# Kernel tuning notes

Measured on AMD Instinct MI355X. Metric: run time of the kernel, lower is better.

## Reference

```python
import jax, jax.numpy as jnp
import numpy as np

HC = 4
C = 2048
TMAX = 8
RMS_EPS = 1e-6
PRE_EPS = 1e-4
SINK_EPS = 1e-6
POST_MULT = 2.0


def setup_inputs() -> dict:
    key = jax.random.key(0)
    k1, k2, k3 = jax.random.split(key, 3)
    B, S = 2, 2048
    x = jax.random.normal(k1, (B, S, HC, C), dtype=jnp.float32)
    phi = jax.random.normal(k2, (HC * C, HC * HC + 2 * HC), dtype=jnp.float32) * 0.02
    b = jnp.zeros((HC * HC + 2 * HC,), dtype=jnp.float32)
    alpha_pre = jnp.ones((), dtype=jnp.float32)
    alpha_post = jnp.ones((), dtype=jnp.float32)
    alpha_res = jnp.ones((), dtype=jnp.float32)
    W = jax.random.normal(k3, (C, C), dtype=jnp.float32) * 0.02
    Wb = jnp.zeros((C,), dtype=jnp.float32)
    return {"x": x, "phi": phi, "b": b, "alpha_pre": alpha_pre,
            "alpha_post": alpha_post, "alpha_res": alpha_res, "W": W, "Wb": Wb}


def _coeffs(x, phi, b, alpha_pre, alpha_post, alpha_res):
    # x: [..., hc, c] -> flatten streams, RMSNorm over k = hc*c
    lead = x.shape[:-2]
    flat = x.reshape(lead + (HC * C,))
    xn = flat * jax.lax.rsqrt(jnp.mean(flat * flat, axis=-1, keepdims=True) + RMS_EPS)
    logits = xn @ phi + b  # [..., hc*hc + 2*hc]
    pre = logits[..., :HC]
    post = logits[..., HC:2 * HC]
    res = logits[..., 2 * HC:].reshape(lead + (HC, HC))
    h_pre = jax.nn.sigmoid(alpha_pre * pre) + PRE_EPS          # [..., hc]
    h_post = POST_MULT * jax.nn.sigmoid(alpha_post * post)     # [..., hc]
    # Sinkhorn normalization -> approximately doubly-stochastic hc x hc matrix
    M = jnp.exp(alpha_res * res)

    def step(m, _):
        m = m / (jnp.sum(m, axis=-1, keepdims=True) + SINK_EPS)
        m = m / (jnp.sum(m, axis=-2, keepdims=True) + SINK_EPS)
        return m, None

    h_res, _ = jax.lax.scan(step, M, None, length=TMAX)
    return h_pre, h_post, h_res


def reference(x, phi, b, alpha_pre, alpha_post, alpha_res, W, Wb):
    xf = x.astype(jnp.float32)
    h_pre, h_post, h_res = _coeffs(xf, phi, b, alpha_pre, alpha_post, alpha_res)
    # combine streams into single layer input: [..., c]
    x_in = jnp.sum(xf * h_pre[..., None], axis=-2)
    f_out = x_in @ W + Wb  # the wrapped layer (Linear)
    # residual stream mixing + broadcasted post-scaled layer output
    x_out = jnp.einsum('...oi,...ic->...oc', h_res, xf) + h_post[..., None] * f_out[..., None, :]
    return x_out.astype(x.dtype)
```

## Files before the change

### kernel.cpp

```cpp
#include <hip/hip_runtime.h>
#include <hip/hip_bf16.h>

#define HCn 4
#define Cn 2048
#define Dn (HCn*Cn)
#define NLg 24
#define TMAXn 8

typedef short bf16x8 __attribute__((ext_vector_type(8)));
typedef float f32x4 __attribute__((ext_vector_type(4)));

__device__ __forceinline__ unsigned int pk2(float a, float b) {
  union { __hip_bfloat162 h; unsigned int u; } v;
  v.h = __float22bfloat162_rn(float2{a, b});
  return v.u;
}
__device__ __forceinline__ float sigm(float z) { return 1.0f / (1.0f + expf(-z)); }

__device__ __forceinline__ void gload_lds16(const void* g, void* l) {
  __builtin_amdgcn_global_load_lds((__attribute__((address_space(1))) void*)(g),
                                   (__attribute__((address_space(3))) void*)(l),
                                   16, 0, 0);
}

__global__ __launch_bounds__(128) void phib_kernel(const float* __restrict__ phi,
                                                   unsigned short* __restrict__ phiB) {
  int tid = threadIdx.x;
  int nt = tid >> 6, lane = tid & 63;
  int ks = blockIdx.x;
  int col = nt * 16 + (lane & 15);
  int kb = ks * 32 + (lane >> 4) * 8;
  float v[8];
#pragma unroll
  for (int e = 0; e < 8; ++e)
    v[e] = (col < NLg) ? phi[(size_t)(kb + e) * NLg + col] : 0.f;
  uint4 o = { pk2(v[0], v[1]), pk2(v[2], v[3]), pk2(v[4], v[5]), pk2(v[6], v[7]) };
  *(uint4*)&phiB[((size_t)(ks * 2 + nt) * 64 + lane) * 8] = o;
}

__global__ __launch_bounds__(512) void logits_kernel(
    const float* __restrict__ x, const unsigned short* __restrict__ phiB,
    float* __restrict__ pbuf) {
  __shared__ float lgp[8][16][33];
  __shared__ float ssp[8][16];

  int tid = threadIdx.x, lane = tid & 63, wid = tid >> 6;
  int g = blockIdx.x >> 2;
  int kc = blockIdx.x & 3;
  long t0 = (long)g * 16;
  int l15 = lane & 15, kg = lane >> 4;

  int kbase = kc * 2048 + wid * 256;
  const float* xr = x + (size_t)(t0 + l15) * Dn + kbase + kg * 8;
  const bf16x8* pB = (const bf16x8*)phiB + (size_t)(kbase >> 5) * 128 + lane;

  float ss = 0.f;
  f32x4 acc0 = {0.f,0.f,0.f,0.f}, acc1 = {0.f,0.f,0.f,0.f};

  float4 A0[3], A1[3]; bf16x8 Bv0[3], Bv1[3];
#define LOADIT(IT, S) {                          \
    A0[S] = *(const float4*)(xr + (IT) * 32);    \
    A1[S] = *(const float4*)(xr + (IT) * 32 + 4);\
    Bv0[S] = pB[(IT) * 128];                     \
    Bv1[S] = pB[(IT) * 128 + 64]; }
#define PROCIT(S) {                                                           \
    float4 P0 = A0[S], P1 = A1[S];                                            \
    ss += P0.x*P0.x + P0.y*P0.y + P0.z*P0.z + P0.w*P0.w;                      \
    ss += P1.x*P1.x + P1.y*P1.y + P1.z*P1.z + P1.w*P1.w;                      \
    uint4 u_ = { pk2(P0.x,P0.y), pk2(P0.z,P0.w), pk2(P1.x,P1.y), pk2(P1.z,P1.w) }; \
    bf16x8 a_ = *(bf16x8*)&u_;                                                \
    acc0 = __builtin_amdgcn_mfma_f32_16x16x32_bf16(a_, Bv0[S], acc0, 0, 0, 0);\
    acc1 = __builtin_amdgcn_mfma_f32_16x16x32_bf16(a_, Bv1[S], acc1, 0, 0, 0); }

  LOADIT(0, 0); LOADIT(1, 1);
#pragma unroll
  for (int it = 0; it < 8; ++it) {
    if (it < 6) LOADIT(it + 2, (it + 2) % 3);
    PROCIT(it % 3);
  }
#undef LOADIT
#undef PROCIT

  ss += __shfl_xor(ss, 16); ss += __shfl_xor(ss, 32);
  if (kg == 0) ssp[wid][l15] = ss;
#pragma unroll
  for (int e = 0; e < 4; ++e) {
    int tok = kg * 4 + e;
    lgp[wid][tok][l15] = acc0[e];
    lgp[wid][tok][16 + l15] = acc1[e];
  }
  __syncthreads();

  for (int q = tid; q < 16 * 25; q += 512) {
    int tk = q / 25, j = q % 25;
    float v = 0.f;
    if (j < 24) {
#pragma unroll
      for (int w = 0; w < 8; ++w) v += lgp[w][tk][j];
    } else {
#pragma unroll
      for (int w = 0; w < 8; ++w) v += ssp[w][tk];
    }
    pbuf[(size_t)(t0 + tk) * 100 + kc * 25 + j] = v;
  }
}

__global__ __launch_bounds__(256) void finalize_kernel(
    const float* __restrict__ pbuf, const float* __restrict__ bb,
    const float* __restrict__ apre_p, const float* __restrict__ apost_p,
    const float* __restrict__ ares_p, float* __restrict__ hpre,
    float* __restrict__ hpost, float* __restrict__ hres) {
  long t = (long)blockIdx.x * 256 + threadIdx.x;
  const float* pt = pbuf + (size_t)t * 100;
  float lg[25];
#pragma unroll
  for (int j = 0; j < 25; ++j)
    lg[j] = pt[j] + pt[25 + j] + pt[50 + j] + pt[75 + j];
  float r = rsqrtf(lg[24] / (float)Dn + 1e-6f);
  float apre = apre_p[0], apost = apost_p[0], ares = ares_p[0];
#pragma unroll
  for (int j = 0; j < NLg; ++j) lg[j] = r * lg[j] + bb[j];
#pragma unroll
  for (int j = 0; j < 4; ++j) hpre[t * 4 + j] = sigm(apre * lg[j]) + 1e-4f;
#pragma unroll
  for (int j = 0; j < 4; ++j) hpost[t * 4 + j] = 2.0f * sigm(apost * lg[4 + j]);
  float m[16];
#pragma unroll
  for (int q = 0; q < 16; ++q) m[q] = expf(ares * lg[8 + q]);
  for (int it = 0; it < TMAXn; ++it) {
#pragma unroll
    for (int o = 0; o < 4; ++o) {
      float rs = m[o*4] + m[o*4+1] + m[o*4+2] + m[o*4+3] + 1e-6f;
      m[o*4] /= rs; m[o*4+1] /= rs; m[o*4+2] /= rs; m[o*4+3] /= rs;
    }
#pragma unroll
    for (int i = 0; i < 4; ++i) {
      float cs = m[i] + m[4+i] + m[8+i] + m[12+i] + 1e-6f;
      m[i] /= cs; m[4+i] /= cs; m[8+i] /= cs; m[12+i] /= cs;
    }
  }
#pragma unroll
  for (int q = 0; q < 16; ++q) hres[t * 16 + q] = m[q];
}

__global__ __launch_bounds__(256) void xin_kernel(
    const float* __restrict__ x, const float* __restrict__ hpre,
    unsigned int* __restrict__ xin) {
  long t = blockIdx.x;
  int tid = threadIdx.x;
  float h0 = hpre[t * 4 + 0], h1 = hpre[t * 4 + 1];
  float h2 = hpre[t * 4 + 2], h3 = hpre[t * 4 + 3];
  const float4* xt = (const float4*)(x + (size_t)t * Dn);
  uint2* xo = (uint2*)xin + (size_t)t * (Cn / 4);
#pragma unroll
  for (int it = 0; it < 2; ++it) {
    int c4 = it * 256 + tid;
    float4 v0 = xt[c4];
    float4 v1 = xt[c4 + 512];
    float4 v2 = xt[c4 + 1024];
    float4 v3 = xt[c4 + 1536];
    float sx = h0*v0.x + h1*v1.x + h2*v2.x + h3*v3.x;
    float sy = h0*v0.y + h1*v1.y + h2*v2.y + h3*v3.y;
    float sz = h0*v0.z + h1*v1.z + h2*v2.z + h3*v3.z;
    float sw = h0*v0.w + h1*v1.w + h2*v2.w + h3*v3.w;
    uint2 o; o.x = pk2(sx, sy); o.y = pk2(sz, sw);
    xo[c4] = o;
  }
}

__global__ __launch_bounds__(256) void wtrans_kernel(const float* __restrict__ W,
                                                     unsigned short* __restrict__ Wt) {
  __shared__ float tile[64][65];
  int kb = blockIdx.y * 64, nb = blockIdx.x * 64;
  int tr = threadIdx.x >> 4;
  int tc = threadIdx.x & 15;
#pragma unroll
  for (int rr = 0; rr < 64; rr += 16) {
    float4 v = *(const float4*)&W[(size_t)(kb + tr + rr) * Cn + nb + tc * 4];
    tile[tr + rr][tc * 4 + 0] = v.x; tile[tr + rr][tc * 4 + 1] = v.y;
    tile[tr + rr][tc * 4 + 2] = v.z; tile[tr + rr][tc * 4 + 3] = v.w;
  }
  __syncthreads();
#pragma unroll
  for (int rr = 0; rr < 64; rr += 16) {
    int n = nb + tr + rr;
    uint2 o;
    o.x = pk2(tile[tc * 4 + 0][tr + rr], tile[tc * 4 + 1][tr + rr]);
    o.y = pk2(tile[tc * 4 + 2][tr + rr], tile[tc * 4 + 3][tr + rr]);
    *(uint2*)&Wt[(size_t)n * Cn + kb + tc * 4] = o;
  }
}

#define BMt 128
#define BNt 128
#define BKt 32
#define GK Cn
__global__ __launch_bounds__(256) void gemm_ep_kernel(
    const unsigned short* __restrict__ xin, const unsigned short* __restrict__ Wt,
    const float* __restrict__ x, const float* __restrict__ Wb,
    const float* __restrict__ hpost, const float* __restrict__ hres,
    float* __restrict__ out) {
  __shared__ __align__(16) unsigned short As[BMt * BKt];
  __shared__ __align__(16) unsigned short Bs[BNt * BKt];
  int tid = threadIdx.x;
  int lane = tid & 63, wid = tid >> 6;
  int wr = wid >> 1, wc = wid & 1;
  int l15 = lane & 15, l4 = lane >> 4;
  int wg = blockIdx.x;
  wg = (wg & 7) * 64 + (wg >> 3);
  int bx = wg & 15, by = wg >> 4;

  f32x4 acc[4][4];
#pragma unroll
  for (int i = 0; i < 4; ++i)
#pragma unroll
    for (int j = 0; j < 4; ++j) acc[i][j] = {0.f, 0.f, 0.f, 0.f};

  const char* Ab = (const char*)xin + (size_t)by * BMt * GK * 2;
  const char* Bb = (const char*)Wt + (size_t)bx * BNt * GK * 2;
  int off0 = tid * 16, off1 = tid * 16 + 4096;
  int row0 = off0 >> 6, colb0 = off0 & 63;
  int row1 = off1 >> 6, colb1 = off1 & 63;

  for (int k0 = 0; k0 < GK; k0 += BKt) {
    gload_lds16(Ab + (size_t)row0 * (GK * 2) + k0 * 2 + colb0, (char*)As + off0);
    gload_lds16(Ab + (size_t)row1 * (GK * 2) + k0 * 2 + colb1, (char*)As + off1);
    gload_lds16(Bb + (size_t)row0 * (GK * 2) + k0 * 2 + colb0, (char*)Bs + off0);
    gload_lds16(Bb + (size_t)row1 * (GK * 2) + k0 * 2 + colb1, (char*)Bs + off1);
    __syncthreads();
    bf16x8 af[4], bfv[4];
#pragma unroll
    for (int fm = 0; fm < 4; ++fm)
      af[fm] = *(const bf16x8*)&As[(wr * 64 + fm * 16 + l15) * BKt + l4 * 8];
#pragma unroll
    for (int fn = 0; fn < 4; ++fn)
      bfv[fn] = *(const bf16x8*)&Bs[(wc * 64 + fn * 16 + l15) * BKt + l4 * 8];
#pragma unroll
    for (int fm = 0; fm < 4; ++fm)
#pragma unroll
      for (int fn = 0; fn < 4; ++fn)
        acc[fm][fn] = __builtin_amdgcn_mfma_f32_16x16x32_bf16(af[fm], bfv[fn], acc[fm][fn], 0, 0, 0);
    __syncthreads();
  }

  int m0 = by * BMt + wr * 64;
  int n0 = bx * BNt + wc * 64;
#pragma unroll
  for (int fm = 0; fm < 4; ++fm) {
#pragma unroll
    for (int e = 0; e < 4; ++e) {
      int t = m0 + fm * 16 + l4 * 4 + e;
      const float* hr = hres + (size_t)t * 16;
      const float* hq = hpost + (size_t)t * 4;
      const float* xt = x + (size_t)t * Dn;
      float* ot = out + (size_t)t * Dn;
      float hr_[16], hq_[4];
#pragma unroll
      for (int q = 0; q < 16; ++q) hr_[q] = hr[q];
#pragma unroll
      for (int q = 0; q < 4; ++q) hq_[q] = hq[q];
#pragma unroll
      for (int fn = 0; fn < 4; ++fn) {
        int c = n0 + fn * 16 + l15;
        float f = acc[fm][fn][e] + Wb[c];
        float x0 = xt[c], x1 = xt[Cn + c], x2 = xt[2 * Cn + c], x3 = xt[3 * Cn + c];
#pragma unroll
        for (int o = 0; o < 4; ++o) {
          ot[(size_t)o * Cn + c] =
              hq_[o] * f + hr_[o*4+0] * x0 + hr_[o*4+1] * x1 + hr_[o*4+2] * x2 + hr_[o*4+3] * x3;
        }
      }
    }
  }
}

extern "C" void kernel_launch(void* const* d_in, const int* in_sizes, int n_in,
                              void* d_out, int out_size, void* d_ws, size_t ws_size,
                              hipStream_t stream) {
  const float* x     = (const float*)d_in[0];
  const float* phi   = (const float*)d_in[1];
  const float* b     = (const float*)d_in[2];
  const float* apre  = (const float*)d_in[3];
  const float* apost = (const float*)d_in[4];
  const float* ares  = (const float*)d_in[5];
  const float* W     = (const float*)d_in[6];
  const float* Wb    = (const float*)d_in[7];
  float* out = (float*)d_out;

  int NT = in_sizes[0] / Dn;
  char* ws = (char*)d_ws;
  size_t off = 0;
  unsigned int*   xin  = (unsigned int*)(ws + off);   off += (size_t)NT * Cn * 2;
  unsigned short* Wt   = (unsigned short*)(ws + off); off += (size_t)Cn * Cn * 2;
  float* hpre  = (float*)(ws + off); off += (size_t)NT * 4 * 4;
  float* hpost = (float*)(ws + off); off += (size_t)NT * 4 * 4;
  float* hres  = (float*)(ws + off); off += (size_t)NT * 16 * 4;
  unsigned short* phiB = (unsigned short*)(ws + off); off += (size_t)Dn * 32 * 2;
  float* pbuf  = (float*)(ws + off); off += (size_t)NT * 100 * 4;

  hipLaunchKernelGGL(phib_kernel, dim3(Dn / 32), dim3(128), 0, stream, phi, phiB);
  hipLaunchKernelGGL(logits_kernel, dim3((NT / 16) * 4), dim3(512), 0, stream,
                     x, phiB, pbuf);
  hipLaunchKernelGGL(finalize_kernel, dim3(NT / 256), dim3(256), 0, stream,
                     pbuf, b, apre, apost, ares, hpre, hpost, hres);
  hipLaunchKernelGGL(xin_kernel, dim3(NT), dim3(256), 0, stream, x, hpre, xin);
  hipLaunchKernelGGL(wtrans_kernel, dim3(Cn / 64, Cn / 64), dim3(256), 0, stream, W, Wt);
  hipLaunchKernelGGL(gemm_ep_kernel, dim3((Cn / BNt) * (NT / BMt)), dim3(256), 0, stream,
                     (const unsigned short*)xin, Wt, x, Wb, hpost, hres, out);
}
```

Measured before the change: 164.3 us.

## Split GEMM and residual-mixing epilogue into separate kernels with bf16 intermediate

The fused GEMM epilogue, which read x and wrote out with strided scalar accesses, is replaced by a plain GEMM that writes bf16 f_out to a workspace buffer. A separate per-token epilogue kernel then reads x and f with float4/uint2 vectorized loads and writes out coalesced. This is meant to remove the poorly coalesced scattered epilogue traffic, at the cost of an extra launch, an extra round trip of f through memory, and bf16 rounding of f_out. The old fused path is kept as a fallback when the workspace is too small.

```diff
diff --git a/kernel.cpp b/kernel.cpp
--- a/kernel.cpp
+++ b/kernel.cpp
@@ -14,6 +14,16 @@
   union { __hip_bfloat162 h; unsigned int u; } v;
   v.h = __float22bfloat162_rn(float2{a, b});
   return v.u;
+}
+__device__ __forceinline__ unsigned short f2bfu(float a) {
+  union { __hip_bfloat16 h; unsigned short u; } v;
+  v.h = __float2bfloat16(a);
+  return v.u;
+}
+__device__ __forceinline__ float bf2f(unsigned int u16) {
+  union { float f; unsigned int x; } v;
+  v.x = u16 << 16;
+  return v.f;
 }
 __device__ __forceinline__ float sigm(float z) { return 1.0f / (1.0f + expf(-z)); }
 
@@ -195,6 +205,103 @@
 #define BNt 128
 #define BKt 32
 #define GK Cn
+__global__ __launch_bounds__(256) void gemm_kernel(
+    const unsigned short* __restrict__ xin, const unsigned short* __restrict__ Wt,
+    const float* __restrict__ Wb, unsigned short* __restrict__ f) {
+  __shared__ __align__(16) unsigned short As[BMt * BKt];
+  __shared__ __align__(16) unsigned short Bs[BNt * BKt];
+  int tid = threadIdx.x;
+  int lane = tid & 63, wid = tid >> 6;
+  int wr = wid >> 1, wc = wid & 1;
+  int l15 = lane & 15, l4 = lane >> 4;
+  int wg = blockIdx.x;
+  wg = (wg & 7) * 64 + (wg >> 3);
+  int bx = wg & 15, by = wg >> 4;
+
+  f32x4 acc[4][4];
+#pragma unroll
+  for (int i = 0; i < 4; ++i)
+#pragma unroll
+    for (int j = 0; j < 4; ++j) acc[i][j] = {0.f, 0.f, 0.f, 0.f};
+
+  const char* Ab = (const char*)xin + (size_t)by * BMt * GK * 2;
+  const char* Bb = (const char*)Wt + (size_t)bx * BNt * GK * 2;
+  int off0 = tid * 16, off1 = tid * 16 + 4096;
+  int row0 = off0 >> 6, colb0 = off0 & 63;
+  int row1 = off1 >> 6, colb1 = off1 & 63;
+
+  for (int k0 = 0; k0 < GK; k0 += BKt) {
+    gload_lds16(Ab + (size_t)row0 * (GK * 2) + k0 * 2 + colb0, (char*)As + off0);
+    gload_lds16(Ab + (size_t)row1 * (GK * 2) + k0 * 2 + colb1, (char*)As + off1);
+    gload_lds16(Bb + (size_t)row0 * (GK * 2) + k0 * 2 + colb0, (char*)Bs + off0);
+    gload_lds16(Bb + (size_t)row1 * (GK * 2) + k0 * 2 + colb1, (char*)Bs + off1);
+    __syncthreads();
+    bf16x8 af[4], bfv[4];
+#pragma unroll
+    for (int fm = 0; fm < 4; ++fm)
+      af[fm] = *(const bf16x8*)&As[(wr * 64 + fm * 16 + l15) * BKt + l4 * 8];
+#pragma unroll
+    for (int fn = 0; fn < 4; ++fn)
+      bfv[fn] = *(const bf16x8*)&Bs[(wc * 64 + fn * 16 + l15) * BKt + l4 * 8];
+#pragma unroll
+    for (int fm = 0; fm < 4; ++fm)
+#pragma unroll
+      for (int fn = 0; fn < 4; ++fn)
+        acc[fm][fn] = __builtin_amdgcn_mfma_f32_16x16x32_bf16(af[fm], bfv[fn], acc[fm][fn], 0, 0, 0);
+    __syncthreads();
+  }
+
+  int m0 = by * BMt + wr * 64;
+  int n0 = bx * BNt + wc * 64;
+#pragma unroll
+  for (int fm = 0; fm < 4; ++fm) {
+#pragma unroll
+    for (int e = 0; e < 4; ++e) {
+      int t = m0 + fm * 16 + l4 * 4 + e;
+      unsigned short* ft = f + (size_t)t * Cn;
+#pragma unroll
+      for (int fn = 0; fn < 4; ++fn) {
+        int c = n0 + fn * 16 + l15;
+        ft[c] = f2bfu(acc[fm][fn][e] + Wb[c]);
+      }
+    }
+  }
+}
+
+__global__ __launch_bounds__(256) void epilogue_kernel(
+    const float* __restrict__ x, const unsigned short* __restrict__ f,
+    const float* __restrict__ hpost, const float* __restrict__ hres,
+    float* __restrict__ out) {
+  long t = blockIdx.x;
+  int tid = threadIdx.x;
+  float hq[4], hr[16];
+#pragma unroll
+  for (int o = 0; o < 4; ++o) hq[o] = hpost[t * 4 + o];
+#pragma unroll
+  for (int q = 0; q < 16; ++q) hr[q] = hres[t * 16 + q];
+  const float4* xt = (const float4*)(x + (size_t)t * Dn);
+  const uint2* ft = (const uint2*)(f + (size_t)t * Cn);
+  float* ot = out + (size_t)t * Dn;
+#pragma unroll
+  for (int it = 0; it < 2; ++it) {
+    int c4 = it * 256 + tid;
+    float4 x0 = xt[c4], x1 = xt[c4 + 512], x2 = xt[c4 + 1024], x3 = xt[c4 + 1536];
+    uint2 fu = ft[c4];
+    float4 fv = { bf2f(fu.x & 0xffffu), bf2f(fu.x >> 16),
+                  bf2f(fu.y & 0xffffu), bf2f(fu.y >> 16) };
+#pragma unroll
+    for (int o = 0; o < 4; ++o) {
+      float a = hr[o*4+0], b = hr[o*4+1], c = hr[o*4+2], d = hr[o*4+3], q = hq[o];
+      float4 r;
+      r.x = q*fv.x + a*x0.x + b*x1.x + c*x2.x + d*x3.x;
+      r.y = q*fv.y + a*x0.y + b*x1.y + c*x2.y + d*x3.y;
+      r.z = q*fv.z + a*x0.z + b*x1.z + c*x2.z + d*x3.z;
+      r.w = q*fv.w + a*x0.w + b*x1.w + c*x2.w + d*x3.w;
+      *(float4*)&ot[(size_t)o * Cn + c4 * 4] = r;
+    }
+  }
+}
+
 __global__ __launch_bounds__(256) void gemm_ep_kernel(
     const unsigned short* __restrict__ xin, const unsigned short* __restrict__ Wt,
     const float* __restrict__ x, const float* __restrict__ Wb,
@@ -262,12 +369,12 @@
 #pragma unroll
       for (int fn = 0; fn < 4; ++fn) {
         int c = n0 + fn * 16 + l15;
-        float f = acc[fm][fn][e] + Wb[c];
+        float fo = acc[fm][fn][e] + Wb[c];
         float x0 = xt[c], x1 = xt[Cn + c], x2 = xt[2 * Cn + c], x3 = xt[3 * Cn + c];
 #pragma unroll
         for (int o = 0; o < 4; ++o) {
           ot[(size_t)o * Cn + c] =
-              hq_[o] * f + hr_[o*4+0] * x0 + hr_[o*4+1] * x1 + hr_[o*4+2] * x2 + hr_[o*4+3] * x3;
+              hq_[o] * fo + hr_[o*4+0] * x0 + hr_[o*4+1] * x1 + hr_[o*4+2] * x2 + hr_[o*4+3] * x3;
         }
       }
     }
@@ -297,6 +404,8 @@
   float* hres  = (float*)(ws + off); off += (size_t)NT * 16 * 4;
   unsigned short* phiB = (unsigned short*)(ws + off); off += (size_t)Dn * 32 * 2;
   float* pbuf  = (float*)(ws + off); off += (size_t)NT * 100 * 4;
+  unsigned short* fbuf = (unsigned short*)(ws + off);
+  size_t off_with_f = off + (size_t)NT * Cn * 2;
 
   hipLaunchKernelGGL(phib_kernel, dim3(Dn / 32), dim3(128), 0, stream, phi, phiB);
   hipLaunchKernelGGL(logits_kernel, dim3((NT / 16) * 4), dim3(512), 0, stream,
@@ -305,6 +414,14 @@
                      pbuf, b, apre, apost, ares, hpre, hpost, hres);
   hipLaunchKernelGGL(xin_kernel, dim3(NT), dim3(256), 0, stream, x, hpre, xin);
   hipLaunchKernelGGL(wtrans_kernel, dim3(Cn / 64, Cn / 64), dim3(256), 0, stream, W, Wt);
-  hipLaunchKernelGGL(gemm_ep_kernel, dim3((Cn / BNt) * (NT / BMt)), dim3(256), 0, stream,
-                     (const unsigned short*)xin, Wt, x, Wb, hpost, hres, out);
-}
+
+  if (ws_size >= off_with_f) {
+    hipLaunchKernelGGL(gemm_kernel, dim3((Cn / BNt) * (NT / BMt)), dim3(256), 0, stream,
+                       (const unsigned short*)xin, Wt, Wb, fbuf);
+    hipLaunchKernelGGL(epilogue_kernel, dim3(NT), dim3(256), 0, stream,
+                       x, fbuf, hpost, hres, out);
+  } else {
+    hipLaunchKernelGGL(gemm_ep_kernel, dim3((Cn / BNt) * (NT / BMt)), dim3(256), 0, stream,
+                       (const unsigned short*)xin, Wt, x, Wb, hpost, hres, out);
+  }
+}
```

Result: no change. 165.8 us (+0.9%).

## Cache bf16 copy of x and split GEMM epilogue into streaming kernel

Applied to the files above, without the earlier changes.

The logits kernel now writes a bf16 copy of x while it converts it for the MFMA. The xin kernel and a new separate epilogue kernel read that half-size copy instead of re-reading the fp32 x. The GEMM now writes f (bias included) as bf16, and a dedicated per-token kernel performs the residual mixing with coalesced vector stores. The aim is to cut fp32 traffic for x and to replace the strided scattered epilogue in the GEMM. The cost is an extra launch, an extra bf16 round trip for f, and reduced precision on the residual term, since x is now rounded to bf16 there.

```diff
diff --git a/kernel.cpp b/kernel.cpp
--- a/kernel.cpp
+++ b/kernel.cpp
@@ -14,6 +14,22 @@
   union { __hip_bfloat162 h; unsigned int u; } v;
   v.h = __float22bfloat162_rn(float2{a, b});
   return v.u;
+}
+__device__ __forceinline__ unsigned short f2bfu(float a) {
+  union { __hip_bfloat16 h; unsigned short u; } v;
+  v.h = __float2bfloat16(a);
+  return v.u;
+}
+__device__ __forceinline__ float bf2f(unsigned int u16) {
+  union { float f; unsigned int x; } v;
+  v.x = u16 << 16;
+  return v.f;
+}
+__device__ __forceinline__ void unpack8(uint4 v, float* o) {
+  o[0] = bf2f(v.x & 0xffffu); o[1] = bf2f(v.x >> 16);
+  o[2] = bf2f(v.y & 0xffffu); o[3] = bf2f(v.y >> 16);
+  o[4] = bf2f(v.z & 0xffffu); o[5] = bf2f(v.z >> 16);
+  o[6] = bf2f(v.w & 0xffffu); o[7] = bf2f(v.w >> 16);
 }
 __device__ __forceinline__ float sigm(float z) { return 1.0f / (1.0f + expf(-z)); }
 
@@ -40,7 +56,7 @@
 
 __global__ __launch_bounds__(512) void logits_kernel(
     const float* __restrict__ x, const unsigned short* __restrict__ phiB,
-    float* __restrict__ pbuf) {
+    float* __restrict__ pbuf, unsigned int* __restrict__ xbf) {
   __shared__ float lgp[8][16][33];
   __shared__ float ssp[8][16];
 
@@ -52,6 +68,7 @@
 
   int kbase = kc * 2048 + wid * 256;
   const float* xr = x + (size_t)(t0 + l15) * Dn + kbase + kg * 8;
+  uint4* xw4 = (uint4*)xbf + ((size_t)(t0 + l15) * 1024 + (kbase >> 3) + kg);
   const bf16x8* pB = (const bf16x8*)phiB + (size_t)(kbase >> 5) * 128 + lane;
 
   float ss = 0.f;
@@ -63,11 +80,12 @@
     A1[S] = *(const float4*)(xr + (IT) * 32 + 4);\
     Bv0[S] = pB[(IT) * 128];                     \
     Bv1[S] = pB[(IT) * 128 + 64]; }
-#define PROCIT(S) {                                                           \
+#define PROCIT(S, IT) {                                                       \
     float4 P0 = A0[S], P1 = A1[S];                                            \
     ss += P0.x*P0.x + P0.y*P0.y + P0.z*P0.z + P0.w*P0.w;                      \
     ss += P1.x*P1.x + P1.y*P1.y + P1.z*P1.z + P1.w*P1.w;                      \
     uint4 u_ = { pk2(P0.x,P0.y), pk2(P0.z,P0.w), pk2(P1.x,P1.y), pk2(P1.z,P1.w) }; \
+    xw4[(IT) * 4] = u_;                                                       \
     bf16x8 a_ = *(bf16x8*)&u_;                                                \
     acc0 = __builtin_amdgcn_mfma_f32_16x16x32_bf16(a_, Bv0[S], acc0, 0, 0, 0);\
     acc1 = __builtin_amdgcn_mfma_f32_16x16x32_bf16(a_, Bv1[S], acc1, 0, 0, 0); }
@@ -76,7 +94,7 @@
 #pragma unroll
   for (int it = 0; it < 8; ++it) {
     if (it < 6) LOADIT(it + 2, (it + 2) % 3);
-    PROCIT(it % 3);
+    PROCIT(it % 3, it);
   }
 #undef LOADIT
 #undef PROCIT
@@ -144,28 +162,21 @@
 }
 
 __global__ __launch_bounds__(256) void xin_kernel(
-    const float* __restrict__ x, const float* __restrict__ hpre,
+    const unsigned int* __restrict__ xbf, const float* __restrict__ hpre,
     unsigned int* __restrict__ xin) {
   long t = blockIdx.x;
   int tid = threadIdx.x;
   float h0 = hpre[t * 4 + 0], h1 = hpre[t * 4 + 1];
   float h2 = hpre[t * 4 + 2], h3 = hpre[t * 4 + 3];
-  const float4* xt = (const float4*)(x + (size_t)t * Dn);
-  uint2* xo = (uint2*)xin + (size_t)t * (Cn / 4);
-#pragma unroll
-  for (int it = 0; it < 2; ++it) {
-    int c4 = it * 256 + tid;
-    float4 v0 = xt[c4];
-    float4 v1 = xt[c4 + 512];
-    float4 v2 = xt[c4 + 1024];
-    float4 v3 = xt[c4 + 1536];
-    float sx = h0*v0.x + h1*v1.x + h2*v2.x + h3*v3.x;
-    float sy = h0*v0.y + h1*v1.y + h2*v2.y + h3*v3.y;
-    float sz = h0*v0.z + h1*v1.z + h2*v2.z + h3*v3.z;
-    float sw = h0*v0.w + h1*v1.w + h2*v2.w + h3*v3.w;
-    uint2 o; o.x = pk2(sx, sy); o.y = pk2(sz, sw);
-    xo[c4] = o;
-  }
+  const uint4* xb = (const uint4*)xbf + (size_t)t * 1024;
+  uint4 v0 = xb[tid], v1 = xb[256 + tid], v2 = xb[512 + tid], v3 = xb[768 + tid];
+  float X0[8], X1[8], X2[8], X3[8];
+  unpack8(v0, X0); unpack8(v1, X1); unpack8(v2, X2); unpack8(v3, X3);
+  float s[8];
+#pragma unroll
+  for (int e = 0; e < 8; ++e) s[e] = h0*X0[e] + h1*X1[e] + h2*X2[e] + h3*X3[e];
+  uint4 o = { pk2(s[0], s[1]), pk2(s[2], s[3]), pk2(s[4], s[5]), pk2(s[6], s[7]) };
+  ((uint4*)xin)[(size_t)t * 256 + tid] = o;
 }
 
 __global__ __launch_bounds__(256) void wtrans_kernel(const float* __restrict__ W,
@@ -195,11 +206,9 @@
 #define BNt 128
 #define BKt 32
 #define GK Cn
-__global__ __launch_bounds__(256) void gemm_ep_kernel(
+__global__ __launch_bounds__(256) void gemm_kernel(
     const unsigned short* __restrict__ xin, const unsigned short* __restrict__ Wt,
-    const float* __restrict__ x, const float* __restrict__ Wb,
-    const float* __restrict__ hpost, const float* __restrict__ hres,
-    float* __restrict__ out) {
+    const float* __restrict__ Wb, unsigned short* __restrict__ f) {
   __shared__ __align__(16) unsigned short As[BMt * BKt];
   __shared__ __align__(16) unsigned short Bs[BNt * BKt];
   int tid = threadIdx.x;
@@ -250,27 +259,46 @@
 #pragma unroll
     for (int e = 0; e < 4; ++e) {
       int t = m0 + fm * 16 + l4 * 4 + e;
-      const float* hr = hres + (size_t)t * 16;
-      const float* hq = hpost + (size_t)t * 4;
-      const float* xt = x + (size_t)t * Dn;
-      float* ot = out + (size_t)t * Dn;
-      float hr_[16], hq_[4];
-#pragma unroll
-      for (int q = 0; q < 16; ++q) hr_[q] = hr[q];
-#pragma unroll
-      for (int q = 0; q < 4; ++q) hq_[q] = hq[q];
+      unsigned short* ft = f + (size_t)t * Cn;
 #pragma unroll
       for (int fn = 0; fn < 4; ++fn) {
         int c = n0 + fn * 16 + l15;
-        float f = acc[fm][fn][e] + Wb[c];
-        float x0 = xt[c], x1 = xt[Cn + c], x2 = xt[2 * Cn + c], x3 = xt[3 * Cn + c];
-#pragma unroll
-        for (int o = 0; o < 4; ++o) {
-          ot[(size_t)o * Cn + c] =
-              hq_[o] * f + hr_[o*4+0] * x0 + hr_[o*4+1] * x1 + hr_[o*4+2] * x2 + hr_[o*4+3] * x3;
-        }
+        ft[c] = f2bfu(acc[fm][fn][e] + Wb[c]);
       }
     }
+  }
+}
+
+__global__ __launch_bounds__(256) void epilogue_kernel(
+    const unsigned int* __restrict__ xbf, const unsigned short* __restrict__ f,
+    const float* __restrict__ hpost, const float* __restrict__ hres,
+    float* __restrict__ out) {
+  long t = blockIdx.x;
+  int tid = threadIdx.x;
+  float hq[4], hr[16];
+#pragma unroll
+  for (int o = 0; o < 4; ++o) hq[o] = hpost[t * 4 + o];
+#pragma unroll
+  for (int q = 0; q < 16; ++q) hr[q] = hres[t * 16 + q];
+  const uint4* xb = (const uint4*)xbf + (size_t)t * 1024;
+  const uint4* fb = (const uint4*)f + (size_t)t * 256;
+  float* ot = out + (size_t)t * Dn;
+
+  uint4 v0 = xb[tid], v1 = xb[256 + tid], v2 = xb[512 + tid], v3 = xb[768 + tid];
+  uint4 fv = fb[tid];
+  float X0[8], X1[8], X2[8], X3[8], F[8];
+  unpack8(v0, X0); unpack8(v1, X1); unpack8(v2, X2); unpack8(v3, X3);
+  unpack8(fv, F);
+#pragma unroll
+  for (int o = 0; o < 4; ++o) {
+    float a = hr[o*4+0], b = hr[o*4+1], c = hr[o*4+2], d = hr[o*4+3], q = hq[o];
+    float r[8];
+#pragma unroll
+    for (int e = 0; e < 8; ++e)
+      r[e] = q*F[e] + a*X0[e] + b*X1[e] + c*X2[e] + d*X3[e];
+    float4* po = (float4*)&ot[(size_t)o * Cn + tid * 8];
+    po[0] = float4{r[0], r[1], r[2], r[3]};
+    po[1] = float4{r[4], r[5], r[6], r[7]};
   }
 }
 
@@ -297,14 +325,18 @@
   float* hres  = (float*)(ws + off); off += (size_t)NT * 16 * 4;
   unsigned short* phiB = (unsigned short*)(ws + off); off += (size_t)Dn * 32 * 2;
   float* pbuf  = (float*)(ws + off); off += (size_t)NT * 100 * 4;
+  unsigned short* fbuf = (unsigned short*)(ws + off); off += (size_t)NT * Cn * 2;
+  unsigned int* xbf    = (unsigned int*)(ws + off);   off += (size_t)NT * Dn * 2;
 
   hipLaunchKernelGGL(phib_kernel, dim3(Dn / 32), dim3(128), 0, stream, phi, phiB);
   hipLaunchKernelGGL(logits_kernel, dim3((NT / 16) * 4), dim3(512), 0, stream,
-                     x, phiB, pbuf);
+                     x, phiB, pbuf, xbf);
   hipLaunchKernelGGL(finalize_kernel, dim3(NT / 256), dim3(256), 0, stream,
                      pbuf, b, apre, apost, ares, hpre, hpost, hres);
-  hipLaunchKernelGGL(xin_kernel, dim3(NT), dim3(256), 0, stream, x, hpre, xin);
+  hipLaunchKernelGGL(xin_kernel, dim3(NT), dim3(256), 0, stream, xbf, hpre, xin);
   hipLaunchKernelGGL(wtrans_kernel, dim3(Cn / 64, Cn / 64), dim3(256), 0, stream, W, Wt);
-  hipLaunchKernelGGL(gemm_ep_kernel, dim3((Cn / BNt) * (NT / BMt)), dim3(256), 0, stream,
-                     (const unsigned short*)xin, Wt, x, Wb, hpost, hres, out);
-}
+  hipLaunchKernelGGL(gemm_kernel, dim3((Cn / BNt) * (NT / BMt)), dim3(256), 0, stream,
+                     (const unsigned short*)xin, Wt, Wb, fbuf);
+  hipLaunchKernelGGL(epilogue_kernel, dim3(NT), dim3(256), 0, stream,
+                     xbf, fbuf, hpost, hres, out);
+}
```

Measured after the change: 174.2 us. +6.0%, slower.

## Double-buffer swizzled GEMM and split residual-mix epilogue into a coalesced kernel

Applied to the files above, without the earlier changes.

The GEMM now uses BK=64 with double-buffered LDS tiles, XOR-swizzled addressing and prefetch of the next k-tile while MFMAs run. This aims to hide global-load latency and reduce LDS bank conflicts. The fused epilogue, which did strided scalar reads of x and scalar writes of out, moves into a separate per-token kernel with float4 loads and nontemporal stores. The GEMM output f is stored as bf16 in an intermediate buffer, which adds an extra round trip through memory and rounding error on f.

```diff
diff --git a/kernel.cpp b/kernel.cpp
--- a/kernel.cpp
+++ b/kernel.cpp
@@ -14,6 +14,16 @@
   union { __hip_bfloat162 h; unsigned int u; } v;
   v.h = __float22bfloat162_rn(float2{a, b});
   return v.u;
+}
+__device__ __forceinline__ unsigned short f2bfu(float a) {
+  union { __hip_bfloat16 h; unsigned short u; } v;
+  v.h = __float2bfloat16(a);
+  return v.u;
+}
+__device__ __forceinline__ float bf2f(unsigned int u16) {
+  union { float f; unsigned int x; } v;
+  v.x = u16 << 16;
+  return v.f;
 }
 __device__ __forceinline__ float sigm(float z) { return 1.0f / (1.0f + expf(-z)); }
 
@@ -193,19 +203,17 @@
 
 #define BMt 128
 #define BNt 128
-#define BKt 32
+#define BKt 64
 #define GK Cn
-__global__ __launch_bounds__(256) void gemm_ep_kernel(
+__global__ __launch_bounds__(256) void gemm_kernel(
     const unsigned short* __restrict__ xin, const unsigned short* __restrict__ Wt,
-    const float* __restrict__ x, const float* __restrict__ Wb,
-    const float* __restrict__ hpost, const float* __restrict__ hres,
-    float* __restrict__ out) {
-  __shared__ __align__(16) unsigned short As[BMt * BKt];
-  __shared__ __align__(16) unsigned short Bs[BNt * BKt];
+    const float* __restrict__ Wb, unsigned short* __restrict__ f) {
+  __shared__ __align__(16) unsigned short As[2][BMt * BKt];
+  __shared__ __align__(16) unsigned short Bs[2][BNt * BKt];
   int tid = threadIdx.x;
   int lane = tid & 63, wid = tid >> 6;
   int wr = wid >> 1, wc = wid & 1;
-  int l15 = lane & 15, l4 = lane >> 4;
+  int l15 = lane & 15, kg = lane >> 4;
   int wg = blockIdx.x;
   wg = (wg & 7) * 64 + (wg >> 3);
   int bx = wg & 15, by = wg >> 4;
@@ -216,31 +224,63 @@
 #pragma unroll
     for (int j = 0; j < 4; ++j) acc[i][j] = {0.f, 0.f, 0.f, 0.f};
 
-  const char* Ab = (const char*)xin + (size_t)by * BMt * GK * 2;
-  const char* Bb = (const char*)Wt + (size_t)bx * BNt * GK * 2;
-  int off0 = tid * 16, off1 = tid * 16 + 4096;
-  int row0 = off0 >> 6, colb0 = off0 & 63;
-  int row1 = off1 >> 6, colb1 = off1 & 63;
-
-  for (int k0 = 0; k0 < GK; k0 += BKt) {
-    gload_lds16(Ab + (size_t)row0 * (GK * 2) + k0 * 2 + colb0, (char*)As + off0);
-    gload_lds16(Ab + (size_t)row1 * (GK * 2) + k0 * 2 + colb1, (char*)As + off1);
-    gload_lds16(Bb + (size_t)row0 * (GK * 2) + k0 * 2 + colb0, (char*)Bs + off0);
-    gload_lds16(Bb + (size_t)row1 * (GK * 2) + k0 * 2 + colb1, (char*)Bs + off1);
-    __syncthreads();
-    bf16x8 af[4], bfv[4];
-#pragma unroll
-    for (int fm = 0; fm < 4; ++fm)
-      af[fm] = *(const bf16x8*)&As[(wr * 64 + fm * 16 + l15) * BKt + l4 * 8];
-#pragma unroll
-    for (int fn = 0; fn < 4; ++fn)
-      bfv[fn] = *(const bf16x8*)&Bs[(wc * 64 + fn * 16 + l15) * BKt + l4 * 8];
-#pragma unroll
-    for (int fm = 0; fm < 4; ++fm)
+  const char* Ab = (const char*)xin + (size_t)by * BMt * (GK * 2);
+  const char* Bb = (const char*)Wt + (size_t)bx * BNt * (GK * 2);
+
+  int soff[4]; size_t sgl[4];
+#pragma unroll
+  for (int i = 0; i < 4; ++i) {
+    int off = tid * 16 + i * 4096;
+    int row = off >> 7, col = off & 127;
+    int scol = col ^ ((row & 7) << 4);
+    soff[i] = off;
+    sgl[i] = (size_t)row * (GK * 2) + scol;
+  }
+#define STAGEG(BUF, K0) {                                                      \
+    _Pragma("unroll")                                                          \
+    for (int i_ = 0; i_ < 4; ++i_)                                             \
+      gload_lds16(Ab + sgl[i_] + (size_t)(K0) * 2, (char*)As[BUF] + soff[i_]); \
+    _Pragma("unroll")                                                          \
+    for (int i_ = 0; i_ < 4; ++i_)                                             \
+      gload_lds16(Bb + sgl[i_] + (size_t)(K0) * 2, (char*)Bs[BUF] + soff[i_]); }
+
+  int aoff[4][2], boff[4][2];
+#pragma unroll
+  for (int fm = 0; fm < 4; ++fm) {
+    int ar = wr * 64 + fm * 16 + l15;
+    int br = wc * 64 + fm * 16 + l15;
+#pragma unroll
+    for (int ks = 0; ks < 2; ++ks) {
+      int c = ks * 64 + kg * 16;
+      aoff[fm][ks] = ar * 128 + (c ^ ((ar & 7) << 4));
+      boff[fm][ks] = br * 128 + (c ^ ((br & 7) << 4));
+    }
+  }
+
+  STAGEG(0, 0);
+  asm volatile("s_waitcnt vmcnt(0)" ::: "memory");
+  __builtin_amdgcn_s_barrier();
+
+  for (int t = 0; t < GK / BKt; ++t) {
+    int cur = t & 1;
+    if (t < GK / BKt - 1) STAGEG(cur ^ 1, (t + 1) * BKt);
+#pragma unroll
+    for (int ks = 0; ks < 2; ++ks) {
+      bf16x8 av[4], bv[4];
+#pragma unroll
+      for (int fm = 0; fm < 4; ++fm)
+        av[fm] = *(const bf16x8*)((const char*)As[cur] + aoff[fm][ks]);
 #pragma unroll
       for (int fn = 0; fn < 4; ++fn)
-        acc[fm][fn] = __builtin_amdgcn_mfma_f32_16x16x32_bf16(af[fm], bfv[fn], acc[fm][fn], 0, 0, 0);
-    __syncthreads();
+        bv[fn] = *(const bf16x8*)((const char*)Bs[cur] + boff[fn][ks]);
+#pragma unroll
+      for (int fm = 0; fm < 4; ++fm)
+#pragma unroll
+        for (int fn = 0; fn < 4; ++fn)
+          acc[fm][fn] = __builtin_amdgcn_mfma_f32_16x16x32_bf16(av[fm], bv[fn], acc[fm][fn], 0, 0, 0);
+    }
+    asm volatile("s_waitcnt vmcnt(0)" ::: "memory");
+    __builtin_amdgcn_s_barrier();
   }
 
   int m0 = by * BMt + wr * 64;
@@ -249,27 +289,47 @@
   for (int fm = 0; fm < 4; ++fm) {
 #pragma unroll
     for (int e = 0; e < 4; ++e) {
-      int t = m0 + fm * 16 + l4 * 4 + e;
-      const float* hr = hres + (size_t)t * 16;
-      const float* hq = hpost + (size_t)t * 4;
-      const float* xt = x + (size_t)t * Dn;
-      float* ot = out + (size_t)t * Dn;
-      float hr_[16], hq_[4];
-#pragma unroll
-      for (int q = 0; q < 16; ++q) hr_[q] = hr[q];
-#pragma unroll
-      for (int q = 0; q < 4; ++q) hq_[q] = hq[q];
+      int t = m0 + fm * 16 + kg * 4 + e;
+      unsigned short* ft = f + (size_t)t * Cn;
 #pragma unroll
       for (int fn = 0; fn < 4; ++fn) {
         int c = n0 + fn * 16 + l15;
-        float f = acc[fm][fn][e] + Wb[c];
-        float x0 = xt[c], x1 = xt[Cn + c], x2 = xt[2 * Cn + c], x3 = xt[3 * Cn + c];
-#pragma unroll
-        for (int o = 0; o < 4; ++o) {
-          ot[(size_t)o * Cn + c] =
-              hq_[o] * f + hr_[o*4+0] * x0 + hr_[o*4+1] * x1 + hr_[o*4+2] * x2 + hr_[o*4+3] * x3;
-        }
+        ft[c] = f2bfu(acc[fm][fn][e] + Wb[c]);
       }
+    }
+  }
+}
+
+__global__ __launch_bounds__(256) void epilogue_kernel(
+    const float* __restrict__ x, const unsigned short* __restrict__ f,
+    const float* __restrict__ hpost, const float* __restrict__ hres,
+    float* __restrict__ out) {
+  long t = blockIdx.x;
+  int tid = threadIdx.x;
+  float hq[4], hr[16];
+#pragma unroll
+  for (int o = 0; o < 4; ++o) hq[o] = hpost[t * 4 + o];
+#pragma unroll
+  for (int q = 0; q < 16; ++q) hr[q] = hres[t * 16 + q];
+  const float4* xt = (const float4*)(x + (size_t)t * Dn);
+  const uint2* ft = (const uint2*)(f + (size_t)t * Cn);
+  float* ot = out + (size_t)t * Dn;
+#pragma unroll
+  for (int it = 0; it < 2; ++it) {
+    int c4 = it * 256 + tid;
+    float4 x0 = xt[c4], x1 = xt[c4 + 512], x2 = xt[c4 + 1024], x3 = xt[c4 + 1536];
+    uint2 fu = ft[c4];
+    float4 fv = { bf2f(fu.x & 0xffffu), bf2f(fu.x >> 16),
+                  bf2f(fu.y & 0xffffu), bf2f(fu.y >> 16) };
+#pragma unroll
+    for (int o = 0; o < 4; ++o) {
+      float a = hr[o*4+0], b = hr[o*4+1], c = hr[o*4+2], d = hr[o*4+3], q = hq[o];
+      f32x4 r;
+      r[0] = q*fv.x + a*x0.x + b*x1.x + c*x2.x + d*x3.x;
+      r[1] = q*fv.y + a*x0.y + b*x1.y + c*x2.y + d*x3.y;
+      r[2] = q*fv.z + a*x0.z + b*x1.z + c*x2.z + d*x3.z;
+      r[3] = q*fv.w + a*x0.w + b*x1.w + c*x2.w + d*x3.w;
+      __builtin_nontemporal_store(r, (f32x4*)&ot[(size_t)o * Cn + c4 * 4]);
     }
   }
 }
@@ -297,6 +357,7 @@
   float* hres  = (float*)(ws + off); off += (size_t)NT * 16 * 4;
   unsigned short* phiB = (unsigned short*)(ws + off); off += (size_t)Dn * 32 * 2;
   float* pbuf  = (float*)(ws + off); off += (size_t)NT * 100 * 4;
+  unsigned short* fbuf = (unsigned short*)(ws + off); off += (size_t)NT * Cn * 2;
 
   hipLaunchKernelGGL(phib_kernel, dim3(Dn / 32), dim3(128), 0, stream, phi, phiB);
   hipLaunchKernelGGL(logits_kernel, dim3((NT / 16) * 4), dim3(512), 0, stream,
@@ -305,6 +366,8 @@
                      pbuf, b, apre, apost, ares, hpre, hpost, hres);
   hipLaunchKernelGGL(xin_kernel, dim3(NT), dim3(256), 0, stream, x, hpre, xin);
   hipLaunchKernelGGL(wtrans_kernel, dim3(Cn / 64, Cn / 64), dim3(256), 0, stream, W, Wt);
-  hipLaunchKernelGGL(gemm_ep_kernel, dim3((Cn / BNt) * (NT / BMt)), dim3(256), 0, stream,
-                     (const unsigned short*)xin, Wt, x, Wb, hpost, hres, out);
-}
+  hipLaunchKernelGGL(gemm_kernel, dim3((Cn / BNt) * (NT / BMt)), dim3(256), 0, stream,
+                     (const unsigned short*)xin, Wt, Wb, fbuf);
+  hipLaunchKernelGGL(epilogue_kernel, dim3(NT), dim3(256), 0, stream,
+                     x, fbuf, hpost, hres, out);
+}
```

Measured after the change: 164.2 us, median of 2. No clear change (-0.0%).
